# Performance work log

Hardware: AMD Instinct MI355X
Metric: run time of the kernel (lower is better)

Reference implementation:

```python
import jax, jax.numpy as jnp
import numpy as np

NUM_HEADS = 32
KV_HEADS = 8
HEAD_DIM = 128
ROPE_BASE = 10000.0

def apply_rope(x):
    # x: [B, H, S, D]
    B, H, S, D = x.shape
    inv_freq = 1.0 / (ROPE_BASE ** (jnp.arange(0, D, 2, dtype=jnp.float32) / D))  # [D/2]
    t = jnp.arange(S, dtype=jnp.float32)
    freqs = jnp.einsum('s,d->sd', t, inv_freq)                 # [S, D/2]
    emb = jnp.concatenate([freqs, freqs], axis=-1)             # [S, D]
    cos = jnp.cos(emb)[None, None, :, :].astype(x.dtype)
    sin = jnp.sin(emb)[None, None, :, :].astype(x.dtype)
    x1, x2 = x[..., : D // 2], x[..., D // 2 :]
    rotated = jnp.concatenate([-x2, x1], axis=-1)
    return x * cos + rotated * sin

def setup_inputs() -> dict:
    key = jax.random.key(0)
    ks = jax.random.split(key, 6)
    B, S, H = 1, 2048, 4096
    scale = 1.0 / np.sqrt(H)
    return {
        'hidden_states': jax.random.normal(ks[0], (B, S, H), jnp.float32),
        'attention_mask': jnp.zeros((B, S), jnp.float32),
        'Wq': jax.random.normal(ks[1], (H, NUM_HEADS * HEAD_DIM), jnp.float32) * scale,
        'Wk': jax.random.normal(ks[2], (H, KV_HEADS * HEAD_DIM), jnp.float32) * scale,
        'Wv': jax.random.normal(ks[3], (H, KV_HEADS * HEAD_DIM), jnp.float32) * scale,
        'Wo': jax.random.normal(ks[4], (NUM_HEADS * HEAD_DIM, H), jnp.float32) * scale,
    }

def reference(hidden_states, attention_mask, Wq, Wk, Wv, Wo):
    B, S, _ = hidden_states.shape
    groups = NUM_HEADS // KV_HEADS
    q = (hidden_states @ Wq).reshape(B, S, NUM_HEADS, HEAD_DIM).transpose(0, 2, 1, 3)  # [B,H,S,D]
    k = (hidden_states @ Wk).reshape(B, S, KV_HEADS, HEAD_DIM).transpose(0, 2, 1, 3)   # [B,KV,S,D]
    v = (hidden_states @ Wv).reshape(B, S, KV_HEADS, HEAD_DIM).transpose(0, 2, 1, 3)
    q = apply_rope(q)
    k = apply_rope(k)
    # GQA: repeat kv heads to match query heads
    k = jnp.repeat(k, groups, axis=1)  # [B,H,S,D]
    v = jnp.repeat(v, groups, axis=1)
    scale = 1.0 / jnp.sqrt(jnp.asarray(HEAD_DIM, q.dtype))
    scores = jnp.einsum('bhqd,bhkd->bhqk', q, k) * scale       # [B,H,S,S]
    scores = scores + attention_mask[:, None, None, :]
    attn = jax.nn.softmax(scores, axis=-1)
    out = jnp.einsum('bhqk,bhkd->bhqd', attn, v)               # [B,H,S,D]
    out = out.transpose(0, 2, 1, 3).reshape(B, S, NUM_HEADS * HEAD_DIM)
    return out @ Wo
```

## Files before the change

kernel.cpp:

```cpp
#include <hip/hip_runtime.h>
#include <hip/hip_bf16.h>

typedef __bf16 bf16_t;
typedef __bf16 bf16x8 __attribute__((ext_vector_type(8)));
typedef float f32x4 __attribute__((ext_vector_type(4)));

__device__ __forceinline__ void gload_lds16(const void* g, void* l) {
  __builtin_amdgcn_global_load_lds((const __attribute__((address_space(1))) void*)g,
                                   (__attribute__((address_space(3))) void*)l, 16, 0, 0);
}

__global__ __launch_bounds__(256) void cvt_bf16_kernel(const float* __restrict__ src,
                                                       bf16_t* __restrict__ dst, int n8) {
  int i = blockIdx.x * 256 + threadIdx.x;
  if (i >= n8) return;
  const float4* s4 = (const float4*)src;
  float4 a = s4[2 * i], b = s4[2 * i + 1];
  bf16x8 o;
  o[0] = (bf16_t)a.x; o[1] = (bf16_t)a.y; o[2] = (bf16_t)a.z; o[3] = (bf16_t)a.w;
  o[4] = (bf16_t)b.x; o[5] = (bf16_t)b.y; o[6] = (bf16_t)b.z; o[7] = (bf16_t)b.w;
  *(bf16x8*)(dst + 8 * (size_t)i) = o;
}

__global__ __launch_bounds__(256) void trcvt_kernel(const float* __restrict__ src,
                                                    bf16_t* __restrict__ dst, int R, int C) {
  __shared__ float tile[32][33];
  int c0 = blockIdx.x * 32, r0 = blockIdx.y * 32;
  int tx = threadIdx.x, ty = threadIdx.y;
#pragma unroll
  for (int i = 0; i < 4; ++i)
    tile[ty + i * 8][tx] = src[(size_t)(r0 + ty + i * 8) * C + c0 + tx];
  __syncthreads();
#pragma unroll
  for (int i = 0; i < 4; ++i)
    dst[(size_t)(c0 + ty + i * 8) * R + r0 + tx] = (bf16_t)tile[tx][ty + i * 8];
}

__global__ __launch_bounds__(256) void trcvt_perm_kernel(const float* __restrict__ src,
                                                         bf16_t* __restrict__ dst, int R, int C) {
  __shared__ float tile[32][33];
  int c0 = blockIdx.x * 32, r0 = blockIdx.y * 32;
  int tx = threadIdx.x, ty = threadIdx.y;
#pragma unroll
  for (int i = 0; i < 4; ++i)
    tile[ty + i * 8][tx] = src[(size_t)(r0 + ty + i * 8) * C + c0 + tx];
  __syncthreads();
#pragma unroll
  for (int i = 0; i < 4; ++i) {
    int rc = c0 + ty + i * 8;
    int dd = rc & 127;
    int q = (dd & 15) + ((dd & 16)) + ((dd >> 5) & 1 ? 64 : 0) + ((dd >> 6) ? 32 : 0);
    int r_out = (rc & ~127) | q;
    dst[(size_t)r_out * R + r0 + tx] = (bf16_t)tile[tx][ty + i * 8];
  }
}

__global__ __launch_bounds__(256) void trb_kernel(const bf16_t* __restrict__ src,
                                                  bf16_t* __restrict__ dst, int R, int C) {
  __shared__ bf16_t tile[32][33];
  int c0 = blockIdx.x * 32, r0 = blockIdx.y * 32;
  int tx = threadIdx.x, ty = threadIdx.y;
#pragma unroll
  for (int i = 0; i < 4; ++i)
    tile[ty + i * 8][tx] = src[(size_t)(r0 + ty + i * 8) * C + c0 + tx];
  __syncthreads();
#pragma unroll
  for (int i = 0; i < 4; ++i)
    dst[(size_t)(c0 + ty + i * 8) * R + r0 + tx] = tile[tx][ty + i * 8];
}

__global__ __launch_bounds__(256) void rope_tab_kernel(float* __restrict__ cosT,
                                                       float* __restrict__ sinT) {
  int i = blockIdx.x * 256 + threadIdx.x;
  int s = i >> 6, d = i & 63;
  float ang = (float)s * powf(10000.0f, -(float)d * (1.0f / 64.0f));
  cosT[i] = cosf(ang);
  sinT[i] = sinf(ang);
}

__global__ __launch_bounds__(512, 2) void proj_gemm_kernel(
    const bf16_t* __restrict__ A, const bf16_t* __restrict__ Wqt,
    const bf16_t* __restrict__ Wkvt, const float* __restrict__ cosT,
    const float* __restrict__ sinT, bf16_t* __restrict__ Qb,
    bf16_t* __restrict__ Kb, bf16_t* __restrict__ Vb) {
  constexpr int K = 4096;
  extern __shared__ unsigned char sMem[];
  const int bx = blockIdx.x;
  const int mt = bx & 7, nt = bx >> 3;
  const int bm = mt * 256;
  const bf16_t* Btb = (nt < 16) ? (Wqt + (size_t)nt * 256 * K)
                                : (Wkvt + (size_t)(nt - 16) * 256 * K);

  const int t = threadIdx.x;
  const int rowU = t >> 2;
  const int cole = ((t & 3) * 8) ^ ((rowU & 8) ? 16 : 0);
  const bf16_t* aS = A + (size_t)(bm + rowU) * K + cole;
  const bf16_t* bS = Btb + (size_t)rowU * K + cole;

  const int lane = t & 63, w = t >> 6;
  const int wm = w >> 2, wn = w & 3;
  const int lr = lane & 15, lq = lane >> 4;
  const int colb = (lq * 16) ^ ((lr & 8) ? 32 : 0);

  auto stA = [&](int c, int h, int j) {
    unsigned char* d = sMem + c * 65536 + h * 16384 + t * 16;
    const bf16_t* g = aS + (size_t)h * 128 * K + j * 64;
    gload_lds16(g, d);
    gload_lds16(g + 32, d + 8192);
  };
  auto stB = [&](int c, int h, int j) {
    unsigned char* d = sMem + c * 65536 + 32768 + h * 16384 + t * 16;
    const bf16_t* g = bS + (size_t)h * 128 * K + j * 64;
    gload_lds16(g, d);
    gload_lds16(g + 32, d + 8192);
  };
  auto LA = [&](int c, int half, int mi, int kk) {
    return *(const bf16x8*)(sMem + c * 65536 + wm * 16384 + kk * 8192 +
                            (half * 64 + mi * 16 + lr) * 64 + colb);
  };
  auto LB = [&](int c, int ni, int kk) {
    return *(const bf16x8*)(sMem + c * 65536 + 32768 + (wn >> 1) * 16384 + kk * 8192 +
                            ((wn & 1) * 64 + ni * 16 + lr) * 64 + colb);
  };

  f32x4 acc[8][4];
#pragma unroll
  for (int i = 0; i < 8; ++i)
#pragma unroll
    for (int n = 0; n < 4; ++n) acc[i][n] = f32x4{0.f, 0.f, 0.f, 0.f};

  stA(0, 0, 0); stA(0, 1, 0); stB(0, 0, 0); stB(0, 1, 0);
  stB(1, 0, 1); stB(1, 1, 1);
  asm volatile("s_waitcnt vmcnt(4)" ::: "memory");
  __builtin_amdgcn_s_barrier();
  __builtin_amdgcn_sched_barrier(0);

  bf16x8 af[4][2], bf[2][2], bf2[2][2];
  for (int j = 0; j < 64; ++j) {
    const int c = j & 1, cn = c ^ 1;
    const int jp1 = (j + 1 < 64) ? j + 1 : 63;
    const int jp2 = (j + 2 < 64) ? j + 2 : 63;
#pragma unroll
    for (int mi = 0; mi < 4; ++mi)
#pragma unroll
      for (int kk = 0; kk < 2; ++kk) af[mi][kk] = LA(c, 0, mi, kk);
#pragma unroll
    for (int ni = 0; ni < 2; ++ni)
#pragma unroll
      for (int kk = 0; kk < 2; ++kk) bf[ni][kk] = LB(c, ni, kk);
    stA(cn, 0, jp1);
    __builtin_amdgcn_s_barrier();
    __builtin_amdgcn_sched_barrier(0);
    __builtin_amdgcn_s_setprio(1);
#pragma unroll
    for (int kk = 0; kk < 2; ++kk)
#pragma unroll
      for (int mi = 0; mi < 4; ++mi)
#pragma unroll
        for (int ni = 0; ni < 2; ++ni)
          acc[mi][ni] = __builtin_amdgcn_mfma_f32_16x16x32_bf16(af[mi][kk], bf[ni][kk],
                                                                acc[mi][ni], 0, 0, 0);
    __builtin_amdgcn_s_setprio(0);
    __builtin_amdgcn_sched_barrier(0);
    __builtin_amdgcn_s_barrier();
#pragma unroll
    for (int ni = 0; ni < 2; ++ni)
#pragma unroll
      for (int kk = 0; kk < 2; ++kk) bf2[ni][kk] = LB(c, 2 + ni, kk);
    stA(cn, 1, jp1);
    __builtin_amdgcn_s_barrier();
    __builtin_amdgcn_sched_barrier(0);
    __builtin_amdgcn_s_setprio(1);
#pragma unroll
    for (int kk = 0; kk < 2; ++kk)
#pragma unroll
      for (int mi = 0; mi < 4; ++mi)
#pragma unroll
        for (int ni = 0; ni < 2; ++ni)
          acc[mi][2 + ni] = __builtin_amdgcn_mfma_f32_16x16x32_bf16(af[mi][kk], bf2[ni][kk],
                                                                    acc[mi][2 + ni], 0, 0, 0);
    __builtin_amdgcn_s_setprio(0);
    __builtin_amdgcn_sched_barrier(0);
    __builtin_amdgcn_s_barrier();
#pragma unroll
    for (int mi = 0; mi < 4; ++mi)
#pragma unroll
      for (int kk = 0; kk < 2; ++kk) af[mi][kk] = LA(c, 1, mi, kk);
    stB(c, 0, jp2);
    __builtin_amdgcn_s_barrier();
    __builtin_amdgcn_sched_barrier(0);
    __builtin_amdgcn_s_setprio(1);
#pragma unroll
    for (int kk = 0; kk < 2; ++kk)
#pragma unroll
      for (int mi = 0; mi < 4; ++mi)
#pragma unroll
        for (int ni = 0; ni < 2; ++ni)
          acc[4 + mi][2 + ni] = __builtin_amdgcn_mfma_f32_16x16x32_bf16(
              af[mi][kk], bf2[ni][kk], acc[4 + mi][2 + ni], 0, 0, 0);
    __builtin_amdgcn_s_setprio(0);
    __builtin_amdgcn_sched_barrier(0);
    __builtin_amdgcn_s_barrier();
    stB(c, 1, jp2);
    asm volatile("s_waitcnt vmcnt(4)" ::: "memory");
    __builtin_amdgcn_s_barrier();
    __builtin_amdgcn_sched_barrier(0);
    __builtin_amdgcn_s_setprio(1);
#pragma unroll
    for (int kk = 0; kk < 2; ++kk)
#pragma unroll
      for (int mi = 0; mi < 4; ++mi)
#pragma unroll
        for (int ni = 0; ni < 2; ++ni)
          acc[4 + mi][ni] = __builtin_amdgcn_mfma_f32_16x16x32_bf16(
              af[mi][kk], bf[ni][kk], acc[4 + mi][ni], 0, 0, 0);
    __builtin_amdgcn_s_setprio(0);
    __builtin_amdgcn_sched_barrier(0);
    __builtin_amdgcn_s_barrier();
  }

  if (nt < 20) {
    const bool isQ = nt < 16;
    bf16_t* dst = isQ ? Qb : Kb;
    const int ld = isQ ? 4096 : 1024;
    const int hh = isQ ? (nt * 2 + (wn >> 1)) : ((nt - 16) * 2 + (wn >> 1));
    const float qs = isQ ? 0.08838834764831845f : 1.0f;
    const int dbase = lr + 32 * (wn & 1);
#pragma unroll
    for (int half = 0; half < 2; ++half)
#pragma unroll
      for (int mi = 0; mi < 4; ++mi)
#pragma unroll
        for (int ni = 0; ni < 2; ++ni) {
          int d = dbase + 16 * ni;
#pragma unroll
          for (int r = 0; r < 4; ++r) {
            int srow = bm + wm * 128 + half * 64 + mi * 16 + lq * 4 + r;
            float cv = cosT[srow * 64 + d], sv = sinT[srow * 64 + d];
            float x1 = acc[half * 4 + mi][ni][r], x2 = acc[half * 4 + mi][ni + 2][r];
            dst[(size_t)srow * ld + hh * 128 + d] = (bf16_t)((x1 * cv - x2 * sv) * qs);
            dst[(size_t)srow * ld + hh * 128 + d + 64] = (bf16_t)((x2 * cv + x1 * sv) * qs);
          }
        }
  } else {
    const int col0 = (nt - 20) * 256 + wn * 64;
#pragma unroll
    for (int half = 0; half < 2; ++half)
#pragma unroll
      for (int mi = 0; mi < 4; ++mi)
#pragma unroll
        for (int ni = 0; ni < 4; ++ni)
#pragma unroll
          for (int r = 0; r < 4; ++r) {
            int srow = bm + wm * 128 + half * 64 + mi * 16 + lq * 4 + r;
            Vb[(size_t)srow * 1024 + col0 + ni * 16 + lr] =
                (bf16_t)acc[half * 4 + mi][ni][r];
          }
  }
}

__global__ __launch_bounds__(256, 2) void out_gemm_kernel(
    const bf16_t* __restrict__ A, const bf16_t* __restrict__ B0,
    float* __restrict__ Cout) {
  constexpr int K = 4096;
  constexpr int MT = 16;
  __shared__ alignas(16) unsigned char sAB[32768];
  unsigned char* sA = sAB;
  unsigned char* sB = sAB + 16384;
  const int bx = blockIdx.x;
  const int mt = bx % MT, nt = bx / MT;
  const int bm = mt * 128;
  const bf16_t* Bt = B0 + (size_t)nt * 128 * K;

  const int t = threadIdx.x;
  const int sr = t >> 3;
  const int scol = ((t & 7) ^ (sr & 7)) * 8;
  const bf16_t* aG = A + (size_t)(bm + sr) * K + scol;
  const bf16_t* bG = Bt + (size_t)sr * K + scol;
  unsigned char* aL = sA + t * 16;
  unsigned char* bL = sB + t * 16;

  const int lane = t & 63, w = t >> 6;
  const int lr = lane & 15, lq = lane >> 4;
  const int swz = (lr & 7) << 4;

  f32x4 acc[2][8];
#pragma unroll
  for (int m = 0; m < 2; ++m)
#pragma unroll
    for (int n = 0; n < 8; ++n) acc[m][n] = f32x4{0.f, 0.f, 0.f, 0.f};

  for (int k0 = 0; k0 < K; k0 += 64) {
    __syncthreads();
#pragma unroll
    for (int p = 0; p < 4; ++p) {
      gload_lds16(aG + (size_t)(p * 32) * K + k0, aL + p * 4096);
      gload_lds16(bG + (size_t)(p * 32) * K + k0, bL + p * 4096);
    }
    __syncthreads();
#pragma unroll
    for (int kk = 0; kk < 2; ++kk) {
      bf16x8 af[2], bfr[8];
#pragma unroll
      for (int m = 0; m < 2; ++m)
        af[m] = *(const bf16x8*)(sA + (w * 32 + m * 16 + lr) * 128 +
                                 ((kk * 64 + lq * 16) ^ swz));
#pragma unroll
      for (int n = 0; n < 8; ++n)
        bfr[n] = *(const bf16x8*)(sB + (n * 16 + lr) * 128 +
                                  ((kk * 64 + lq * 16) ^ swz));
#pragma unroll
      for (int m = 0; m < 2; ++m)
#pragma unroll
        for (int n = 0; n < 8; ++n)
          acc[m][n] = __builtin_amdgcn_mfma_f32_16x16x32_bf16(af[m], bfr[n],
                                                              acc[m][n], 0, 0, 0);
    }
  }
#pragma unroll
  for (int m = 0; m < 2; ++m)
#pragma unroll
    for (int n = 0; n < 8; ++n)
#pragma unroll
      for (int r = 0; r < 4; ++r)
        Cout[(size_t)(bm + w * 32 + m * 16 + lq * 4 + r) * 4096 + nt * 128 +
             n * 16 + lr] = acc[m][n][r];
}

__global__ __launch_bounds__(256, 2) void attn_kernel(
    const bf16_t* __restrict__ Qb, const bf16_t* __restrict__ Kb,
    const bf16_t* __restrict__ Vt, const float* __restrict__ mask,
    bf16_t* __restrict__ Ob) {
  extern __shared__ unsigned char sMem[];
  const int bx = blockIdx.x;
  const int h = bx >> 4, qt = bx & 15;
  const int kvh = h >> 2;
  const int q0 = qt * 128;
  const int t = threadIdx.x, lane = t & 63, w = t >> 6;
  const int lr = lane & 15, lq = lane >> 4;
  const int swz = (lr & 7) << 4;

  bf16x8 qf[2][4];
#pragma unroll
  for (int m = 0; m < 2; ++m)
#pragma unroll
    for (int kk = 0; kk < 4; ++kk)
      qf[m][kk] = *(const bf16x8*)(Qb + (size_t)(q0 + w * 32 + m * 16 + lr) * 4096 +
                                   h * 128 + kk * 32 + lq * 8);

  const int srK = t >> 4;
  const int scK = ((t & 15) ^ (srK & 7)) * 8;
  const bf16_t* kG = Kb + (size_t)srK * 1024 + kvh * 128 + scK;
  const int srV = t >> 3;
  const int scV = ((t & 7) ^ (srV & 7)) * 8;
  const bf16_t* vG = Vt + (size_t)(kvh * 128 + srV) * 2048 + scV;

  auto stage = [&](int c, int kt) {
    unsigned char* kL = sMem + c * 16384 + t * 16;
    unsigned char* vL = sMem + 32768 + c * 16384 + t * 16;
#pragma unroll
    for (int p = 0; p < 4; ++p)
      gload_lds16(kG + (size_t)(kt * 64 + p * 16) * 1024, kL + p * 4096);
#pragma unroll
    for (int p = 0; p < 4; ++p)
      gload_lds16(vG + (size_t)(p * 32) * 2048 + kt * 64, vL + p * 4096);
  };

  f32x4 o[2][8];
#pragma unroll
  for (int m = 0; m < 2; ++m)
#pragma unroll
    for (int n = 0; n < 8; ++n) o[m][n] = f32x4{0.f, 0.f, 0.f, 0.f};
  float mrun[2][4], lp[2][4];
#pragma unroll
  for (int m = 0; m < 2; ++m)
#pragma unroll
    for (int r = 0; r < 4; ++r) { mrun[m][r] = -1e30f; lp[m][r] = 0.f; }

  stage(0, 0);
  __syncthreads();

  for (int kt = 0; kt < 32; ++kt) {
    const int cur = kt & 1;
    if (kt < 31) stage(cur ^ 1, kt + 1);
    const unsigned char* sK = sMem + cur * 16384;
    const unsigned char* sV = sMem + 32768 + cur * 16384;
    unsigned char* sPw = sMem + 65536 + w * 4096;

    f32x4 scf[2][4];
#pragma unroll
    for (int m = 0; m < 2; ++m)
#pragma unroll
      for (int n = 0; n < 4; ++n) scf[m][n] = f32x4{0.f, 0.f, 0.f, 0.f};
    __builtin_amdgcn_s_setprio(1);
#pragma unroll
    for (int kk = 0; kk < 4; ++kk)
#pragma unroll
      for (int n = 0; n < 4; ++n) {
        bf16x8 b = *(const bf16x8*)(sK + (n * 16 + lr) * 256 +
                                    ((kk * 64 + lq * 16) ^ swz));
        scf[0][n] = __builtin_amdgcn_mfma_f32_16x16x32_bf16(qf[0][kk], b, scf[0][n], 0, 0, 0);
        scf[1][n] = __builtin_amdgcn_mfma_f32_16x16x32_bf16(qf[1][kk], b, scf[1][n], 0, 0, 0);
      }
    __builtin_amdgcn_s_setprio(0);

    float mk[4];
#pragma unroll
    for (int n = 0; n < 4; ++n) mk[n] = mask[kt * 64 + n * 16 + lr];

    float al[2][4];
#pragma unroll
    for (int m = 0; m < 2; ++m) {
#pragma unroll
      for (int n = 0; n < 4; ++n)
#pragma unroll
        for (int r = 0; r < 4; ++r) scf[m][n][r] += mk[n];
#pragma unroll
      for (int r = 0; r < 4; ++r) {
        float rm = fmaxf(fmaxf(scf[m][0][r], scf[m][1][r]),
                         fmaxf(scf[m][2][r], scf[m][3][r]));
#pragma unroll
        for (int off = 8; off > 0; off >>= 1) rm = fmaxf(rm, __shfl_xor(rm, off));
        float nm = fmaxf(mrun[m][r], rm);
        al[m][r] = __expf(mrun[m][r] - nm);
        mrun[m][r] = nm;
      }
      float ps[4] = {0.f, 0.f, 0.f, 0.f};
#pragma unroll
      for (int n = 0; n < 4; ++n)
#pragma unroll
        for (int r = 0; r < 4; ++r) {
          float p = __expf(scf[m][n][r] - mrun[m][r]);
          scf[m][n][r] = p;
          ps[r] += p;
        }
#pragma unroll
      for (int r = 0; r < 4; ++r) lp[m][r] = lp[m][r] * al[m][r] + ps[r];
#pragma unroll
      for (int n = 0; n < 4; ++n)
#pragma unroll
        for (int r = 0; r < 4; ++r) {
          int prow = lq * 4 + r;
          *(bf16_t*)(sPw + m * 2048 + prow * 128 +
                     (((n * 16 + lr) * 2) ^ ((prow & 7) << 4))) = (bf16_t)scf[m][n][r];
        }
#pragma unroll
      for (int n = 0; n < 8; ++n)
#pragma unroll
        for (int r = 0; r < 4; ++r) o[m][n][r] *= al[m][r];
    }

    bf16x8 pa[2][2];
#pragma unroll
    for (int m = 0; m < 2; ++m)
#pragma unroll
      for (int kk = 0; kk < 2; ++kk)
        pa[m][kk] = *(const bf16x8*)(sPw + m * 2048 + lr * 128 +
                                     ((kk * 64 + lq * 16) ^ swz));
    __builtin_amdgcn_s_setprio(1);
#pragma unroll
    for (int kk = 0; kk < 2; ++kk)
#pragma unroll
      for (int n = 0; n < 8; ++n) {
        bf16x8 vb = *(const bf16x8*)(sV + (n * 16 + lr) * 128 +
                                     ((kk * 64 + lq * 16) ^ swz));
        o[0][n] = __builtin_amdgcn_mfma_f32_16x16x32_bf16(pa[0][kk], vb, o[0][n], 0, 0, 0);
        o[1][n] = __builtin_amdgcn_mfma_f32_16x16x32_bf16(pa[1][kk], vb, o[1][n], 0, 0, 0);
      }
    __builtin_amdgcn_s_setprio(0);
    __syncthreads();
  }

  float inv[2][4];
#pragma unroll
  for (int m = 0; m < 2; ++m)
#pragma unroll
    for (int r = 0; r < 4; ++r) {
      float l = lp[m][r];
#pragma unroll
      for (int off = 8; off > 0; off >>= 1) l += __shfl_xor(l, off);
      inv[m][r] = 1.0f / l;
    }
#pragma unroll
  for (int m = 0; m < 2; ++m)
#pragma unroll
    for (int n = 0; n < 8; ++n)
#pragma unroll
      for (int r = 0; r < 4; ++r)
        Ob[(size_t)(q0 + w * 32 + m * 16 + lq * 4 + r) * 4096 + h * 128 + n * 16 + lr] =
            (bf16_t)(o[m][n][r] * inv[m][r]);
}

extern "C" void kernel_launch(void* const* d_in, const int* in_sizes, int n_in,
                              void* d_out, int out_size, void* d_ws, size_t ws_size,
                              hipStream_t stream) {
  const float* hidden = (const float*)d_in[0];
  const float* mask = (const float*)d_in[1];
  const float* Wq = (const float*)d_in[2];
  const float* Wk = (const float*)d_in[3];
  const float* Wv = (const float*)d_in[4];
  const float* Wo = (const float*)d_in[5];
  float* out = (float*)d_out;
  char* ws = (char*)d_ws;

  bf16_t* hB   = (bf16_t*)(ws + 0);
  bf16_t* Wqt  = (bf16_t*)(ws + 16777216);
  bf16_t* Wkvt = (bf16_t*)(ws + 50331648);
  bf16_t* Wot  = (bf16_t*)(ws + 67108864);
  bf16_t* Qb   = (bf16_t*)(ws + 100663296);
  bf16_t* Kb   = (bf16_t*)(ws + 117440512);
  bf16_t* Vb   = (bf16_t*)(ws + 121634816);
  bf16_t* Vt   = (bf16_t*)(ws + 125829120);
  bf16_t* Ob   = (bf16_t*)(ws + 130023424);
  float*  cosT = (float*)(ws + 146800640);
  float*  sinT = (float*)(ws + 147324928);

  hipFuncSetAttribute((const void*)attn_kernel,
                      hipFuncAttributeMaxDynamicSharedMemorySize, 81920);
  hipFuncSetAttribute((const void*)proj_gemm_kernel,
                      hipFuncAttributeMaxDynamicSharedMemorySize, 131072);

  cvt_bf16_kernel<<<4096, 256, 0, stream>>>(hidden, hB, 1048576);
  trcvt_perm_kernel<<<dim3(128, 128), dim3(32, 8), 0, stream>>>(Wq, Wqt, 4096, 4096);
  trcvt_perm_kernel<<<dim3(32, 128), dim3(32, 8), 0, stream>>>(Wk, Wkvt, 4096, 1024);
  trcvt_kernel<<<dim3(32, 128), dim3(32, 8), 0, stream>>>(Wv, Wkvt + (size_t)1024 * 4096, 4096, 1024);
  trcvt_kernel<<<dim3(128, 128), dim3(32, 8), 0, stream>>>(Wo, Wot, 4096, 4096);
  rope_tab_kernel<<<512, 256, 0, stream>>>(cosT, sinT);
  proj_gemm_kernel<<<192, 512, 131072, stream>>>(hB, Wqt, Wkvt, cosT, sinT, Qb, Kb, Vb);
  trb_kernel<<<dim3(32, 64), dim3(32, 8), 0, stream>>>(Vb, Vt, 2048, 1024);
  attn_kernel<<<512, 256, 81920, stream>>>(Qb, Kb, Vt, mask, Ob);
  out_gemm_kernel<<<512, 256, 0, stream>>>(Ob, Wot, out);
}
```

Before: 352.6 us.

## Rewrite attention with 32x32 MFMA, register-resident P and lazy rescaling

Restructures the attention kernel to use 32x32x16 bf16 MFMAs computing S^T = K·Q^T, so the softmax probabilities stay in registers and are exchanged across half-waves with shuffles instead of round-tripping through LDS. Blocks grow to 512 threads covering 256 query rows, the mask is staged into LDS alongside K/V, and the online-softmax rescale of the output accumulator is skipped unless the running max grows by more than a threshold. This removes LDS traffic for P and cuts per-row reduction work, but it raises register pressure and halves the grid to 256 blocks, which may lower occupancy.

```diff
diff --git a/kernel.cpp b/kernel.cpp
--- a/kernel.cpp
+++ b/kernel.cpp
@@ -3,11 +3,19 @@
 
 typedef __bf16 bf16_t;
 typedef __bf16 bf16x8 __attribute__((ext_vector_type(8)));
+typedef __bf16 bf16x4 __attribute__((ext_vector_type(4)));
 typedef float f32x4 __attribute__((ext_vector_type(4)));
+typedef float f32x16 __attribute__((ext_vector_type(16)));
 
 __device__ __forceinline__ void gload_lds16(const void* g, void* l) {
   __builtin_amdgcn_global_load_lds((const __attribute__((address_space(1))) void*)g,
                                    (__attribute__((address_space(3))) void*)l, 16, 0, 0);
+}
+
+__device__ __forceinline__ unsigned pk_bf16(float a, float b) {
+  unsigned r;
+  asm("v_cvt_pk_bf16_f32 %0, %1, %2" : "=v"(r) : "v"(a), "v"(b));
+  return r;
 }
 
 __global__ __launch_bounds__(256) void cvt_bf16_kernel(const float* __restrict__ src,
@@ -327,168 +335,136 @@
              n * 16 + lr] = acc[m][n][r];
 }
 
-__global__ __launch_bounds__(256, 2) void attn_kernel(
+__global__ __launch_bounds__(512) void attn_kernel(
     const bf16_t* __restrict__ Qb, const bf16_t* __restrict__ Kb,
     const bf16_t* __restrict__ Vt, const float* __restrict__ mask,
     bf16_t* __restrict__ Ob) {
   extern __shared__ unsigned char sMem[];
   const int bx = blockIdx.x;
-  const int h = bx >> 4, qt = bx & 15;
+  const int h = bx >> 3, qt = bx & 7;
   const int kvh = h >> 2;
-  const int q0 = qt * 128;
   const int t = threadIdx.x, lane = t & 63, w = t >> 6;
-  const int lr = lane & 15, lq = lane >> 4;
-  const int swz = (lr & 7) << 4;
-
-  bf16x8 qf[2][4];
-#pragma unroll
-  for (int m = 0; m < 2; ++m)
-#pragma unroll
-    for (int kk = 0; kk < 4; ++kk)
-      qf[m][kk] = *(const bf16x8*)(Qb + (size_t)(q0 + w * 32 + m * 16 + lr) * 4096 +
-                                   h * 128 + kk * 32 + lq * 8);
-
-  const int srK = t >> 4;
-  const int scK = ((t & 15) ^ (srK & 7)) * 8;
-  const bf16_t* kG = Kb + (size_t)srK * 1024 + kvh * 128 + scK;
-  const int srV = t >> 3;
-  const int scV = ((t & 7) ^ (srV & 7)) * 8;
-  const bf16_t* vG = Vt + (size_t)(kvh * 128 + srV) * 2048 + scV;
+  const int ln = lane & 31, hi = lane >> 5;
+  const int q0 = qt * 256 + w * 32;
+  const int swz = (ln & 7) << 4;
+
+  bf16x8 qf[8];
+#pragma unroll
+  for (int ds = 0; ds < 8; ++ds)
+    qf[ds] = *(const bf16x8*)(Qb + (size_t)(q0 + ln) * 4096 + h * 128 + ds * 16 + hi * 8);
+
+  const int krow = t >> 4, kg = t & 15;
+  const bf16_t* kSrc = Kb + (size_t)krow * 1024 + kvh * 128 +
+                       (((kg * 16) ^ ((krow & 7) << 4)) >> 1);
+  const int vrow = t >> 3, vg = t & 7;
+  const bf16_t* vSrc = Vt + (size_t)(kvh * 128 + vrow) * 2048 +
+                       (((vg * 16) ^ ((vrow & 7) << 4)) >> 1);
 
   auto stage = [&](int c, int kt) {
-    unsigned char* kL = sMem + c * 16384 + t * 16;
-    unsigned char* vL = sMem + 32768 + c * 16384 + t * 16;
-#pragma unroll
-    for (int p = 0; p < 4; ++p)
-      gload_lds16(kG + (size_t)(kt * 64 + p * 16) * 1024, kL + p * 4096);
-#pragma unroll
-    for (int p = 0; p < 4; ++p)
-      gload_lds16(vG + (size_t)(p * 32) * 2048 + kt * 64, vL + p * 4096);
+    unsigned char* kD = sMem + c * 16384 + t * 16;
+    unsigned char* vD = sMem + 32768 + c * 16384 + t * 16;
+    gload_lds16(kSrc + (size_t)kt * 64 * 1024, kD);
+    gload_lds16(kSrc + (size_t)(kt * 64 + 32) * 1024, kD + 8192);
+    gload_lds16(vSrc + kt * 64, vD);
+    gload_lds16(vSrc + (size_t)64 * 2048 + kt * 64, vD + 8192);
+    if (t < 16) gload_lds16(mask + kt * 64 + t * 4, sMem + 65536 + c * 256 + t * 16);
   };
 
-  f32x4 o[2][8];
-#pragma unroll
-  for (int m = 0; m < 2; ++m)
-#pragma unroll
-    for (int n = 0; n < 8; ++n) o[m][n] = f32x4{0.f, 0.f, 0.f, 0.f};
-  float mrun[2][4], lp[2][4];
-#pragma unroll
-  for (int m = 0; m < 2; ++m)
-#pragma unroll
-    for (int r = 0; r < 4; ++r) { mrun[m][r] = -1e30f; lp[m][r] = 0.f; }
+  f32x16 o[4];
+#pragma unroll
+  for (int db = 0; db < 4; ++db)
+#pragma unroll
+    for (int e = 0; e < 16; ++e) o[db][e] = 0.f;
+  float mrun = -1e30f, lp = 0.f;
 
   stage(0, 0);
   __syncthreads();
 
   for (int kt = 0; kt < 32; ++kt) {
-    const int cur = kt & 1;
-    if (kt < 31) stage(cur ^ 1, kt + 1);
-    const unsigned char* sK = sMem + cur * 16384;
-    const unsigned char* sV = sMem + 32768 + cur * 16384;
-    unsigned char* sPw = sMem + 65536 + w * 4096;
-
-    f32x4 scf[2][4];
-#pragma unroll
-    for (int m = 0; m < 2; ++m)
-#pragma unroll
-      for (int n = 0; n < 4; ++n) scf[m][n] = f32x4{0.f, 0.f, 0.f, 0.f};
-    __builtin_amdgcn_s_setprio(1);
-#pragma unroll
-    for (int kk = 0; kk < 4; ++kk)
-#pragma unroll
-      for (int n = 0; n < 4; ++n) {
-        bf16x8 b = *(const bf16x8*)(sK + (n * 16 + lr) * 256 +
-                                    ((kk * 64 + lq * 16) ^ swz));
-        scf[0][n] = __builtin_amdgcn_mfma_f32_16x16x32_bf16(qf[0][kk], b, scf[0][n], 0, 0, 0);
-        scf[1][n] = __builtin_amdgcn_mfma_f32_16x16x32_bf16(qf[1][kk], b, scf[1][n], 0, 0, 0);
+    const int c = kt & 1;
+    if (kt < 31) stage(c ^ 1, kt + 1);
+    const unsigned char* sK = sMem + c * 16384;
+    const unsigned char* sV = sMem + 32768 + c * 16384;
+    const unsigned char* sMk = sMem + 65536 + c * 256;
+
+#pragma unroll
+    for (int sub = 0; sub < 2; ++sub) {
+      f32x16 s;
+#pragma unroll
+      for (int e = 0; e < 16; ++e) s[e] = 0.f;
+      __builtin_amdgcn_s_setprio(1);
+#pragma unroll
+      for (int ds = 0; ds < 8; ++ds) {
+        bf16x8 kf = *(const bf16x8*)(sK + (sub * 32 + ln) * 256 +
+                                     ((ds * 32 + hi * 16) ^ swz));
+        s = __builtin_amdgcn_mfma_f32_32x32x16_bf16(kf, qf[ds], s, 0, 0, 0);
       }
-    __builtin_amdgcn_s_setprio(0);
-
-    float mk[4];
-#pragma unroll
-    for (int n = 0; n < 4; ++n) mk[n] = mask[kt * 64 + n * 16 + lr];
-
-    float al[2][4];
-#pragma unroll
-    for (int m = 0; m < 2; ++m) {
-#pragma unroll
-      for (int n = 0; n < 4; ++n)
-#pragma unroll
-        for (int r = 0; r < 4; ++r) scf[m][n][r] += mk[n];
-#pragma unroll
-      for (int r = 0; r < 4; ++r) {
-        float rm = fmaxf(fmaxf(scf[m][0][r], scf[m][1][r]),
-                         fmaxf(scf[m][2][r], scf[m][3][r]));
-#pragma unroll
-        for (int off = 8; off > 0; off >>= 1) rm = fmaxf(rm, __shfl_xor(rm, off));
-        float nm = fmaxf(mrun[m][r], rm);
-        al[m][r] = __expf(mrun[m][r] - nm);
-        mrun[m][r] = nm;
+      __builtin_amdgcn_s_setprio(0);
+#pragma unroll
+      for (int rg = 0; rg < 4; ++rg) {
+        float4 mv = *(const float4*)(sMk + (sub * 32 + rg * 8 + 4 * hi) * 4);
+        s[rg * 4 + 0] += mv.x; s[rg * 4 + 1] += mv.y;
+        s[rg * 4 + 2] += mv.z; s[rg * 4 + 3] += mv.w;
       }
-      float ps[4] = {0.f, 0.f, 0.f, 0.f};
-#pragma unroll
-      for (int n = 0; n < 4; ++n)
-#pragma unroll
-        for (int r = 0; r < 4; ++r) {
-          float p = __expf(scf[m][n][r] - mrun[m][r]);
-          scf[m][n][r] = p;
-          ps[r] += p;
+      float pm = s[0];
+#pragma unroll
+      for (int e = 1; e < 16; ++e) pm = fmaxf(pm, s[e]);
+      pm = fmaxf(pm, __shfl_xor(pm, 32));
+      if (!__all(pm - mrun <= 8.0f)) {
+        float nm = fmaxf(mrun, pm);
+        float al = __expf(mrun - nm);
+        mrun = nm;
+        lp *= al;
+#pragma unroll
+        for (int db = 0; db < 4; ++db)
+#pragma unroll
+          for (int e = 0; e < 16; ++e) o[db][e] *= al;
+      }
+      float p[16], ps = 0.f;
+#pragma unroll
+      for (int e = 0; e < 16; ++e) {
+        p[e] = __expf(s[e] - mrun);
+        ps += p[e];
+      }
+      lp += ps;
+#pragma unroll
+      for (int hh = 0; hh < 2; ++hh) {
+        unsigned w0 = pk_bf16(p[8 * hh + 0], p[8 * hh + 1]);
+        unsigned w1 = pk_bf16(p[8 * hh + 2], p[8 * hh + 3]);
+        unsigned w2 = pk_bf16(p[8 * hh + 4], p[8 * hh + 5]);
+        unsigned w3 = pk_bf16(p[8 * hh + 6], p[8 * hh + 7]);
+        unsigned pw0 = __shfl_xor((int)w0, 32), pw1 = __shfl_xor((int)w1, 32);
+        unsigned pw2 = __shfl_xor((int)w2, 32), pw3 = __shfl_xor((int)w3, 32);
+        union { unsigned u[4]; bf16x8 v; } pf;
+        pf.u[0] = hi ? pw2 : w0;
+        pf.u[1] = hi ? pw3 : w1;
+        pf.u[2] = hi ? w2 : pw0;
+        pf.u[3] = hi ? w3 : pw1;
+        __builtin_amdgcn_s_setprio(1);
+#pragma unroll
+        for (int db = 0; db < 4; ++db) {
+          bf16x8 vf = *(const bf16x8*)(sV + (db * 32 + ln) * 128 +
+                                       ((sub * 64 + hh * 32 + hi * 16) ^ swz));
+          o[db] = __builtin_amdgcn_mfma_f32_32x32x16_bf16(vf, pf.v, o[db], 0, 0, 0);
         }
-#pragma unroll
-      for (int r = 0; r < 4; ++r) lp[m][r] = lp[m][r] * al[m][r] + ps[r];
-#pragma unroll
-      for (int n = 0; n < 4; ++n)
-#pragma unroll
-        for (int r = 0; r < 4; ++r) {
-          int prow = lq * 4 + r;
-          *(bf16_t*)(sPw + m * 2048 + prow * 128 +
-                     (((n * 16 + lr) * 2) ^ ((prow & 7) << 4))) = (bf16_t)scf[m][n][r];
-        }
-#pragma unroll
-      for (int n = 0; n < 8; ++n)
-#pragma unroll
-        for (int r = 0; r < 4; ++r) o[m][n][r] *= al[m][r];
+        __builtin_amdgcn_s_setprio(0);
+      }
     }
-
-    bf16x8 pa[2][2];
-#pragma unroll
-    for (int m = 0; m < 2; ++m)
-#pragma unroll
-      for (int kk = 0; kk < 2; ++kk)
-        pa[m][kk] = *(const bf16x8*)(sPw + m * 2048 + lr * 128 +
-                                     ((kk * 64 + lq * 16) ^ swz));
-    __builtin_amdgcn_s_setprio(1);
-#pragma unroll
-    for (int kk = 0; kk < 2; ++kk)
-#pragma unroll
-      for (int n = 0; n < 8; ++n) {
-        bf16x8 vb = *(const bf16x8*)(sV + (n * 16 + lr) * 128 +
-                                     ((kk * 64 + lq * 16) ^ swz));
-        o[0][n] = __builtin_amdgcn_mfma_f32_16x16x32_bf16(pa[0][kk], vb, o[0][n], 0, 0, 0);
-        o[1][n] = __builtin_amdgcn_mfma_f32_16x16x32_bf16(pa[1][kk], vb, o[1][n], 0, 0, 0);
-      }
-    __builtin_amdgcn_s_setprio(0);
     __syncthreads();
   }
 
-  float inv[2][4];
-#pragma unroll
-  for (int m = 0; m < 2; ++m)
-#pragma unroll
-    for (int r = 0; r < 4; ++r) {
-      float l = lp[m][r];
-#pragma unroll
-      for (int off = 8; off > 0; off >>= 1) l += __shfl_xor(l, off);
-      inv[m][r] = 1.0f / l;
+  float l = lp + __shfl_xor(lp, 32);
+  float inv = 1.0f / l;
+  bf16_t* orow = Ob + (size_t)(q0 + ln) * 4096 + h * 128;
+#pragma unroll
+  for (int db = 0; db < 4; ++db)
+#pragma unroll
+    for (int rg = 0; rg < 4; ++rg) {
+      bf16x4 ov;
+#pragma unroll
+      for (int j = 0; j < 4; ++j) ov[j] = (bf16_t)(o[db][rg * 4 + j] * inv);
+      *(bf16x4*)(orow + db * 32 + rg * 8 + hi * 4) = ov;
     }
-#pragma unroll
-  for (int m = 0; m < 2; ++m)
-#pragma unroll
-    for (int n = 0; n < 8; ++n)
-#pragma unroll
-      for (int r = 0; r < 4; ++r)
-        Ob[(size_t)(q0 + w * 32 + m * 16 + lq * 4 + r) * 4096 + h * 128 + n * 16 + lr] =
-            (bf16_t)(o[m][n][r] * inv[m][r]);
 }
 
 extern "C" void kernel_launch(void* const* d_in, const int* in_sizes, int n_in,
@@ -516,7 +492,7 @@
   float*  sinT = (float*)(ws + 147324928);
 
   hipFuncSetAttribute((const void*)attn_kernel,
-                      hipFuncAttributeMaxDynamicSharedMemorySize, 81920);
+                      hipFuncAttributeMaxDynamicSharedMemorySize, 66560);
   hipFuncSetAttribute((const void*)proj_gemm_kernel,
                       hipFuncAttributeMaxDynamicSharedMemorySize, 131072);
 
@@ -528,6 +504,6 @@
   rope_tab_kernel<<<512, 256, 0, stream>>>(cosT, sinT);
   proj_gemm_kernel<<<192, 512, 131072, stream>>>(hB, Wqt, Wkvt, cosT, sinT, Qb, Kb, Vb);
   trb_kernel<<<dim3(32, 64), dim3(32, 8), 0, stream>>>(Vb, Vt, 2048, 1024);
-  attn_kernel<<<512, 256, 81920, stream>>>(Qb, Kb, Vt, mask, Ob);
+  attn_kernel<<<256, 512, 66560, stream>>>(Qb, Kb, Vt, mask, Ob);
   out_gemm_kernel<<<512, 256, 0, stream>>>(Ob, Wot, out);
 }
```

After: 329.2 us. 6.6% less time.
